# Kernel optimization log

Measured on AMD Instinct MI355X. Metric: run time of the kernel, lower is better.

Reference implementation:

```python
import jax, jax.numpy as jnp
import numpy as np

T, B, D, H = 128, 256, 1024, 150  # seq_len, batch, input feat, lstm hidden (bidir out = 2H = 300)


def _lstm_dir(x, Wih, Whh, b):
    # x: [T,Bn,in]; Wih: [4H,in]; Whh: [4H,H]; b: [4H]. PyTorch gate order i,f,g,o.
    xW = jnp.einsum('tbi,gi->tbg', x, Wih) + b
    Bn = x.shape[1]
    init = (jnp.zeros((Bn, H), x.dtype), jnp.zeros((Bn, H), x.dtype))
    def step(carry, xg):
        h, c = carry
        g = xg + h @ Whh.T
        i, f, gg, o = jnp.split(g, 4, axis=-1)
        c = jax.nn.sigmoid(f) * c + jax.nn.sigmoid(i) * jnp.tanh(gg)
        h = jax.nn.sigmoid(o) * jnp.tanh(c)
        return (h, c), h
    _, hs = jax.lax.scan(step, init, xW)
    return hs


def _bidir(x, Wih, Whh, b):
    fwd = _lstm_dir(x, Wih[0], Whh[0], b[0])
    bwd = _lstm_dir(x[::-1], Wih[1], Whh[1], b[1])[::-1]
    return jnp.concatenate([fwd, bwd], axis=-1)


def _bilstm2(x, Wih0, Whh0, b0, Wih1, Whh1, b1):
    # 2-layer bidirectional LSTM (eval mode, dropout off)
    h = _bidir(x, Wih0, Whh0, b0)
    return _bidir(h, Wih1, Whh1, b1)


def setup_inputs() -> dict:
    key = jax.random.key(0)
    ks = iter(jax.random.split(key, 32))
    U = jax.random.normal(next(ks), (T, B, D), jnp.float32)
    speaker = jax.random.randint(next(ks), (T, B), 0, 2)
    qmask = jax.nn.one_hot(speaker, 2, dtype=jnp.int32)  # [T,B,2] speaker one-hot
    umask = jnp.ones((T, B), jnp.float32)
    seq_lengths = jnp.full((B,), T, dtype=jnp.int32)
    def w(shape):
        return jax.random.normal(next(ks), shape, jnp.float32) * 0.05
    inp = dict(U=U, qmask=qmask, umask=umask, seq_lengths=seq_lengths)
    for pfx in ('rnn', 'pr'):
        inp[pfx + '_Wih0'] = w((2, 4 * H, D))
        inp[pfx + '_Whh0'] = w((2, 4 * H, H))
        inp[pfx + '_b0'] = w((2, 4 * H))
        inp[pfx + '_Wih1'] = w((2, 4 * H, 2 * H))
        inp[pfx + '_Whh1'] = w((2, 4 * H, H))
        inp[pfx + '_b1'] = w((2, 4 * H))
    return inp


def reference(U, qmask, umask, seq_lengths, rnn_Wih0, rnn_Whh0, rnn_b0, rnn_Wih1, rnn_Whh1, rnn_b1, pr_Wih0, pr_Whh0, pr_b0, pr_Wih1, pr_Whh1, pr_b1):
    speaker = jnp.argmax(qmask, axis=-1)  # [T,B] party id of each utterance
    # position of utterance t within its party's compacted sequence
    pos = jnp.take_along_axis(jnp.cumsum(qmask, axis=0), speaker[..., None], axis=-1)[..., 0] - 1  # [T,B]
    bidx = jnp.broadcast_to(jnp.arange(B)[None, :], (T, B))
    # scatter utterances into per-party sequences: [2,T,B,D]
    U_parties = jnp.zeros((2, T, B, D), U.dtype).at[speaker, pos, bidx].set(U)
    xp = jnp.concatenate([U_parties[0], U_parties[1]], axis=1)  # [T,2B,D]
    Ep = _bilstm2(xp, pr_Wih0, pr_Whh0, pr_b0, pr_Wih1, pr_Whh1, pr_b1)  # [T,2B,2H]
    Ep = jnp.stack([Ep[:, :B], Ep[:, B:]], axis=0)  # [2,T,B,2H]
    U_p = Ep[speaker, pos, bidx]  # gather back to dialogue order, [T,B,2H]
    emotions = _bilstm2(U, rnn_Wih0, rnn_Whh0, rnn_b0, rnn_Wih1, rnn_Whh1, rnn_b1)  # [T,B,2H]
    return (emotions + U_p) * umask[..., None]
```

## Files before the change

### kernel.cpp

```cpp
#include <hip/hip_runtime.h>
#include <hip/hip_bf16.h>
#include <math.h>

#define T_ 128
#define B_ 256
#define BP 512
#define D_ 1024
#define H_ 150
#define G_ 600
#define O_ 300
#define ROWS 16
#define NT_ 38
#define KT_ 5
#define KTX 10
#define KAP 40
#define HSTR 168
#define GST 620
#define TPB 512
#define EIT 5
#define NTB 38

typedef float v4f    __attribute__((ext_vector_type(4)));
typedef short bf16x8 __attribute__((ext_vector_type(8)));
typedef float f32x4  __attribute__((ext_vector_type(4)));
typedef unsigned int u32x4 __attribute__((ext_vector_type(4)));
union HU { u32x4 u; bf16x8 h; };

static const size_t N_INV   = 0;
static const size_t N_WPK   = 65536;
static const size_t N_BW1   = N_WPK + 778240;
static const size_t N_HPK   = N_BW1 + 778240;
static const size_t N_X     = N_HPK + 31457280;
static const size_t N_TOTAL = N_X + 78643200 + 256;

static const size_t WPS      = (size_t)NT_ * KT_ * 2 * 512;
static const size_t BW1_STR  = (size_t)KTX * NTB * 2 * 512;
static const size_t BW0_STR  = 32ull * NTB * 2 * 512;
static const size_t RNN_PL   = 2048ull * KAP * 128;
static const size_t PR_PL    = 4096ull * KAP * 128;

static const size_t INV_OFF   = 0;
static const size_t WIHT0_OFF = 65536;
static const size_t WIHT1_OFF = WIHT0_OFF + 4ull * 1024 * 600;
static const size_t WPK_OFF   = WIHT1_OFF + 4ull * 300 * 600;
static const size_t WPK_WORDS = 8ull * NT_ * KT_ * 2 * 512 / 2;
static const size_t XW_OFF    = WPK_OFF + WPK_WORDS;
static const size_t XSLOT     = 32768ull * 600;
static size_t hrnn_off(int nslots) { return XW_OFF + (size_t)nslots * XSLOT; }
static size_t hpr_off(int nslots)  { return hrnn_off(nslots) + 32768ull * 300; }

__device__ __forceinline__ float fsig(float x) {
    return __builtin_amdgcn_rcpf(1.f + __expf(-x));
}
__device__ __forceinline__ float ftanh(float x) {
    float xc = fminf(fmaxf(x, -15.f), 15.f);
    float e = __expf(-2.f * xc);
    return (1.f - e) * __builtin_amdgcn_rcpf(1.f + e);
}

__global__ void k_pos(const int* __restrict__ qmask, int* __restrict__ inv) {
    int b = threadIdx.x;
    for (int p = 0; p < T_; ++p) {
        inv[p * BP + b] = -1;
        inv[p * BP + B_ + b] = -1;
    }
    int c0 = 0, c1 = 0;
    for (int t = 0; t < T_; ++t) {
        int s = qmask[(t * B_ + b) * 2 + 1];
        int p = s ? c1++ : c0++;
        inv[p * BP + s * B_ + b] = t * B_ + b;
    }
}

__global__ void k_zero(unsigned int* __restrict__ p, int n4) {
    int gid = blockIdx.x * 256 + threadIdx.x;
    if (gid < n4) *(u32x4*)(p + (size_t)gid * 4) = (u32x4){0, 0, 0, 0};
}

__global__ void k_transpose(const float* __restrict__ src, float* __restrict__ dst,
                            int K) {
    int idx = blockIdx.x * 256 + threadIdx.x;
    int total = K * G_;
    if (idx < total) {
        int k = idx / G_, g = idx - k * G_;
        dst[idx] = src[(size_t)g * K + k];
    }
}

struct PackArgs { const float* whh[8]; };
__global__ void k_pack(PackArgs pa, unsigned short* __restrict__ wpk) {
    int gid = blockIdx.x * 256 + threadIdx.x;
    int lane = gid & 63;
    int q = gid >> 6;
    int kt = q % KT_; q /= KT_;
    int nt = q % NT_; q /= NT_;
    if (q >= 8) return;
    const float* W = pa.whh[q];
    int col = nt * 16 + (lane & 15);
    int kbase = kt * 32 + (lane >> 4) * 8;
    size_t base = ((((size_t)q * NT_ + nt) * KT_ + kt) * 2) * 512 + (size_t)lane * 8;
    for (int j = 0; j < 8; ++j) {
        int k = kbase + j;
        float v = (col < G_ && k < H_) ? W[(size_t)col * H_ + k] : 0.f;
        unsigned u = __float_as_uint(v);
        unsigned short hi = (unsigned short)(u >> 16);
        float hf = __uint_as_float(u & 0xffff0000u);
        unsigned short lo = (unsigned short)(__float_as_uint(v - hf) >> 16);
        wpk[base + j] = hi;
        wpk[base + 512 + j] = lo;
    }
}

__global__ void k_packB(const float* __restrict__ W, int K, int KT,
                        unsigned short* __restrict__ out) {
    int gid = blockIdx.x * 256 + threadIdx.x;
    int lane = gid & 63, q = gid >> 6;
    int kt = q % KT, nt = q / KT;
    if (nt >= NTB) return;
    int col = nt * 16 + (lane & 15);
    int kb = kt * 32 + (lane >> 4) * 8;
    size_t base = ((size_t)(kt * NTB + nt) * 2) * 512 + (size_t)lane * 8;
    bf16x8 h8 = {0, 0, 0, 0, 0, 0, 0, 0};
    bf16x8 l8 = {0, 0, 0, 0, 0, 0, 0, 0};
#pragma unroll
    for (int j = 0; j < 8; ++j) {
        int k = kb + j;
        float v = (col < G_ && k < K) ? W[(size_t)col * K + k] : 0.f;
        unsigned u = __float_as_uint(v);
        h8[j] = (short)(u >> 16);
        float hf = __uint_as_float(u & 0xffff0000u);
        l8[j] = (short)(__float_as_uint(v - hf) >> 16);
    }
    *(bf16x8*)(out + base) = h8;
    *(bf16x8*)(out + base + 512) = l8;
}

__global__ void k_packU(const float* __restrict__ A, unsigned short* __restrict__ hi,
                        unsigned short* __restrict__ lo) {
    int gid = blockIdx.x * 256 + threadIdx.x;
    int kc = gid & 127, rr = gid >> 7;
    const float* ap = A + (size_t)rr * 1024 + kc * 8;
    size_t off = ((size_t)((rr >> 4) * 128 + kc) * 16 + (rr & 15)) * 8;
    bf16x8 h8, l8;
#pragma unroll
    for (int j = 0; j < 8; ++j) {
        float v = ap[j];
        unsigned u = __float_as_uint(v);
        h8[j] = (short)(u >> 16);
        float hf = __uint_as_float(u & 0xffff0000u);
        l8[j] = (short)(__float_as_uint(v - hf) >> 16);
    }
    *(bf16x8*)(hi + off) = h8;
    *(bf16x8*)(lo + off) = l8;
}

#define LOADK(kt_, S)                                                          \
  {                                                                            \
    if (MODE == 0) {                                                           \
      _Pragma("unroll") for (int mi = 0; mi < 4; ++mi) {                       \
        size_t aoff = ((size_t)((m0 >> 4) + mi) * KA + (kt_) * 4 + quad);      \
        aoff = (aoff * 16 + col16) * 8;                                        \
        a_h##S[mi] = *(const bf16x8*)(Ahi + aoff);                             \
        a_l##S[mi] = *(const bf16x8*)(Alo + aoff);                             \
      }                                                                        \
    } else {                                                                   \
      _Pragma("unroll") for (int mi = 0; mi < 4; ++mi) {                       \
        const unsigned int* ap =                                               \
            Aw + (size_t)(m0 + mi * 16 + col16) * KA + (kt_) * 32 + quad * 8;  \
        u32x4 w0 = *(const u32x4*)ap;                                          \
        u32x4 w1 = *(const u32x4*)(ap + 4);                                    \
        HU hh, ll;                                                             \
        hh.u.x = (w0.x >> 16) | (w0.y & 0xffff0000u);                          \
        hh.u.y = (w0.z >> 16) | (w0.w & 0xffff0000u);                          \
        hh.u.z = (w1.x >> 16) | (w1.y & 0xffff0000u);                          \
        hh.u.w = (w1.z >> 16) | (w1.w & 0xffff0000u);                          \
        ll.u.x = (w0.x & 0xffffu) | (w0.y << 16);                              \
        ll.u.y = (w0.z & 0xffffu) | (w0.w << 16);                              \
        ll.u.z = (w1.x & 0xffffu) | (w1.y << 16);                              \
        ll.u.w = (w1.z & 0xffffu) | (w1.w << 16);                              \
        a_h##S[mi] = hh.h;                                                     \
        a_l##S[mi] = ll.h;                                                     \
      }                                                                        \
    }                                                                          \
    _Pragma("unroll") for (int ni = 0; ni < 4; ++ni) {                         \
      if (bnv[ni]) {                                                           \
        size_t bo = ((size_t)((kt_) * NTB + nt0 + ni) * 2) * 512 + lane * 8;   \
        b_h##S[ni] = *(const bf16x8*)(Bpk + bo);                               \
        b_l##S[ni] = *(const bf16x8*)(Bpk + bo + 512);                         \
      }                                                                        \
    }                                                                          \
  }

#define MMK(S)                                                                 \
  _Pragma("unroll") for (int mi = 0; mi < 4; ++mi)                             \
    _Pragma("unroll") for (int ni = 0; ni < 4; ++ni) {                         \
      acc[mi][ni] = __builtin_amdgcn_mfma_f32_16x16x32_bf16(                   \
          a_h##S[mi], b_h##S[ni], acc[mi][ni], 0, 0, 0);                       \
      acc[mi][ni] = __builtin_amdgcn_mfma_f32_16x16x32_bf16(                   \
          a_h##S[mi], b_l##S[ni], acc[mi][ni], 0, 0, 0);                       \
      acc[mi][ni] = __builtin_amdgcn_mfma_f32_16x16x32_bf16(                   \
          a_l##S[mi], b_h##S[ni], acc[mi][ni], 0, 0, 0);                       \
    }

template<int MODE, int KTN, int KA>
__global__ __launch_bounds__(256) void k_mgemm(const unsigned short* __restrict__ Ahi,
                                               const unsigned short* __restrict__ Alo,
                                               const unsigned int* __restrict__ Aw,
                                               const unsigned short* __restrict__ Bpk,
                                               const float* __restrict__ bias,
                                               float* __restrict__ C) {
    int tid = threadIdx.x, lane = tid & 63, wv = tid >> 6;
    int col16 = lane & 15, quad = lane >> 4;
    int n0 = blockIdx.x * 128 + (wv & 1) * 64;
    int m0 = blockIdx.y * 128 + (wv >> 1) * 64;
    int nt0 = n0 >> 4;

    bool bnv[4]; float bs[4];
#pragma unroll
    for (int ni = 0; ni < 4; ++ni) {
        int nt = nt0 + ni;
        bnv[ni] = (nt < NTB);
        int cc = nt * 16 + col16;
        bs[ni] = (cc < G_) ? bias[cc] : 0.f;
    }

    f32x4 acc[4][4];
#pragma unroll
    for (int mi = 0; mi < 4; ++mi)
#pragma unroll
        for (int ni = 0; ni < 4; ++ni) acc[mi][ni] = (f32x4){0.f, 0.f, 0.f, 0.f};

    bf16x8 z8 = {0, 0, 0, 0, 0, 0, 0, 0};
    bf16x8 a_h0[4], a_l0[4], b_h0[4], b_l0[4];
    bf16x8 a_h1[4], a_l1[4], b_h1[4], b_l1[4];
#pragma unroll
    for (int ni = 0; ni < 4; ++ni) {
        b_h0[ni] = z8; b_l0[ni] = z8; b_h1[ni] = z8; b_l1[ni] = z8;
    }

    LOADK(0, 0);
#pragma unroll 1
    for (int kt = 0; kt < KTN; kt += 2) {
        LOADK(kt + 1, 1);
        MMK(0);
        if (kt + 2 < KTN) { LOADK(kt + 2, 0); }
        MMK(1);
    }

#pragma unroll
    for (int mi = 0; mi < 4; ++mi)
#pragma unroll
        for (int ni = 0; ni < 4; ++ni) {
            int col = n0 + ni * 16 + col16;
            if (col < G_) {
#pragma unroll
                for (int p = 0; p < 4; ++p)
                    C[(size_t)(m0 + mi * 16 + quad * 4 + p) * G_ + col] =
                        acc[mi][ni][p] + bs[ni];
            }
        }
}

__global__ __launch_bounds__(256) void k_gemm(const float* __restrict__ A,
                                              const float* __restrict__ BT,
                                              const float* __restrict__ bias,
                                              float* __restrict__ C,
                                              int M, int K) {
    __shared__ __align__(16) float As[16][136];
    __shared__ __align__(16) float Bs[16][68];
    int n0 = blockIdx.x * 64, m0 = blockIdx.y * 128;
    int tid = threadIdx.x;
    int tx = tid & 15, ty = tid >> 4;
    int ar = tid >> 2, ac = (tid & 3) * 4;
    int kr = tid >> 4, nc = (tid & 15) * 4;
    float acc[8][4];
#pragma unroll
    for (int i = 0; i < 8; ++i)
#pragma unroll
        for (int j = 0; j < 4; ++j) acc[i][j] = 0.f;

    for (int k0 = 0; k0 < K; k0 += 16) {
        bool fullK = (k0 + 16 <= K);
#pragma unroll
        for (int half = 0; half < 2; ++half) {
            int m = m0 + ar + half * 64;
            const float* ap = A + (size_t)m * K + k0 + ac;
            if (fullK) {
                v4f v = *(const v4f*)ap;
                As[ac + 0][ar + half * 64] = v.x;
                As[ac + 1][ar + half * 64] = v.y;
                As[ac + 2][ar + half * 64] = v.z;
                As[ac + 3][ar + half * 64] = v.w;
            } else {
#pragma unroll
                for (int i = 0; i < 4; ++i) {
                    int k = k0 + ac + i;
                    As[ac + i][ar + half * 64] = (k < K) ? ap[i] : 0.f;
                }
            }
        }
        {
            int k = k0 + kr, n = n0 + nc;
            if (fullK && n + 3 < G_) {
                v4f v = *(const v4f*)(BT + (size_t)k * G_ + n);
                Bs[kr][nc + 0] = v.x; Bs[kr][nc + 1] = v.y;
                Bs[kr][nc + 2] = v.z; Bs[kr][nc + 3] = v.w;
            } else {
#pragma unroll
                for (int i = 0; i < 4; ++i) {
                    int nn = n + i;
                    Bs[kr][nc + i] = (k < K && nn < G_) ? BT[(size_t)k * G_ + nn] : 0.f;
                }
            }
        }
        __syncthreads();
#pragma unroll
        for (int kk = 0; kk < 16; ++kk) {
            v4f a0 = *(const v4f*)&As[kk][ty * 8];
            v4f a1 = *(const v4f*)&As[kk][ty * 8 + 4];
            v4f b  = *(const v4f*)&Bs[kk][tx * 4];
            const float* af = (const float*)&a0;
            const float* af2 = (const float*)&a1;
            const float* bf = (const float*)&b;
#pragma unroll
            for (int i = 0; i < 4; ++i)
#pragma unroll
                for (int j = 0; j < 4; ++j) {
                    acc[i][j] += af[i] * bf[j];
                    acc[4 + i][j] += af2[i] * bf[j];
                }
        }
        __syncthreads();
    }
    int n = n0 + tx * 4;
    if (n + 3 < G_) {
        v4f bv = *(const v4f*)(bias + n);
#pragma unroll
        for (int i = 0; i < 8; ++i) {
            int m = m0 + ty * 8 + i;
            v4f o = {acc[i][0] + bv.x, acc[i][1] + bv.y, acc[i][2] + bv.z, acc[i][3] + bv.w};
            *(v4f*)(C + (size_t)m * G_ + n) = o;
        }
    } else {
#pragma unroll
        for (int i = 0; i < 8; ++i) {
            int m = m0 + ty * 8 + i;
#pragma unroll
            for (int j = 0; j < 4; ++j)
                if (n + j < G_) C[(size_t)m * G_ + n + j] = acc[i][j] + bias[n + j];
        }
    }
}

struct Combo0 {
    const float* xw;
    const unsigned short* wpk;
    const float* bias;
    unsigned short* phi;
    unsigned short* plo;
    int Bn, colOff, bwd, gIn;
};
struct Scan0Args { Combo0 c[4]; const int* inv; int blkStart[5]; };

__global__ __launch_bounds__(TPB) void k_scan0(Scan0Args args) {
    int bx = blockIdx.x, ci = 0;
#pragma unroll
    for (int i = 1; i < 4; ++i)
        if (bx >= args.blkStart[i]) ci = i;
    Combo0 cb = args.c[ci];
    int row0 = (bx - args.blkStart[ci]) * ROWS;

    __shared__ __align__(16) unsigned short hsh[ROWS * HSTR];
    __shared__ __align__(16) unsigned short hsl[ROWS * HSTR];
    __shared__ float cs[ROWS * 152];
    __shared__ float gs[ROWS * GST];
    int tid = threadIdx.x;
    int lane = tid & 63, wv = tid >> 6;
    int col16 = lane & 15, quad = lane >> 4;
    for (int i = tid; i < ROWS * HSTR; i += TPB) { hsh[i] = 0; hsl[i] = 0; }
    for (int i = tid; i < ROWS * 152; i += TPB) cs[i] = 0.f;
    __syncthreads();

    int er[EIT], ej[EIT];
#pragma unroll
    for (int it = 0; it < EIT; ++it) {
        int i = tid + it * TPB;
        er[it] = i / 160;
        ej[it] = i - er[it] * 160;
    }

    for (int s = 0; s < T_; ++s) {
        int t = cb.bwd ? (T_ - 1 - s) : s;

        float xi[EIT], xf_[EIT], xg[EIT], xo[EIT];
#pragma unroll
        for (int it = 0; it < EIT; ++it) {
            int r = er[it], j = ej[it];
            const float* xr;
            if (cb.gIn) {
                int g = args.inv[t * cb.Bn + row0 + r];
                xr = (g >= 0) ? cb.xw + (size_t)g * G_ : cb.bias;
            } else {
                xr = cb.xw + ((size_t)t * cb.Bn + row0 + r) * G_;
            }
            bool act = (j < H_);
            xi[it]  = act ? xr[j] : 0.f;
            xf_[it] = act ? xr[H_ + j] : 0.f;
            xg[it]  = act ? xr[2 * H_ + j] : 0.f;
            xo[it]  = act ? xr[3 * H_ + j] : 0.f;
        }

        bf16x8 ahi[KT_], alo[KT_];
#pragma unroll
        for (int kt = 0; kt < KT_; ++kt) {
            int off = col16 * HSTR + kt * 32 + quad * 8;
            ahi[kt] = *(const bf16x8*)&hsh[off];
            alo[kt] = *(const bf16x8*)&hsl[off];
        }

        for (int nt = wv; nt < NT_; nt += 8) {
            f32x4 a0 = {0.f, 0.f, 0.f, 0.f};
            f32x4 a1 = {0.f, 0.f, 0.f, 0.f};
            const bf16x8* bp = (const bf16x8*)cb.wpk + ((size_t)nt * KT_) * 2 * 64 + lane;
#pragma unroll
            for (int kt = 0; kt < KT_; ++kt) {
                bf16x8 bhi = bp[0];
                bf16x8 blo = bp[64];
                bp += 128;
                if (kt < 3) {
                    a0 = __builtin_amdgcn_mfma_f32_16x16x32_bf16(ahi[kt], bhi, a0, 0, 0, 0);
                    a0 = __builtin_amdgcn_mfma_f32_16x16x32_bf16(ahi[kt], blo, a0, 0, 0, 0);
                    a0 = __builtin_amdgcn_mfma_f32_16x16x32_bf16(alo[kt], bhi, a0, 0, 0, 0);
                } else {
                    a1 = __builtin_amdgcn_mfma_f32_16x16x32_bf16(ahi[kt], bhi, a1, 0, 0, 0);
                    a1 = __builtin_amdgcn_mfma_f32_16x16x32_bf16(ahi[kt], blo, a1, 0, 0, 0);
                    a1 = __builtin_amdgcn_mfma_f32_16x16x32_bf16(alo[kt], bhi, a1, 0, 0, 0);
                }
            }
            f32x4 acc = a0 + a1;
#pragma unroll
            for (int p = 0; p < 4; ++p)
                gs[(quad * 4 + p) * GST + nt * 16 + col16] = acc[p];
        }
        __syncthreads();

        size_t mb = ((size_t)t * cb.Bn + row0) >> 4;
#pragma unroll
        for (int it = 0; it < EIT; ++it) {
            int r = er[it], j = ej[it];
            if (j < H_) {
                float gi = gs[r * GST + j] + xi[it];
                float gf = gs[r * GST + H_ + j] + xf_[it];
                float gg = gs[r * GST + 2 * H_ + j] + xg[it];
                float go = gs[r * GST + 3 * H_ + j] + xo[it];
                float ii = fsig(gi), ff = fsig(gf), oo = fsig(go);
                float cc = ff * cs[r * 152 + j] + ii * ftanh(gg);
                float hh = oo * ftanh(cc);
                cs[r * 152 + j] = cc;
                unsigned u = __float_as_uint(hh);
                unsigned short hi16 = (unsigned short)(u >> 16);
                float hf = __uint_as_float(u & 0xffff0000u);
                unsigned short lo16 = (unsigned short)(__float_as_uint(hh - hf) >> 16);
                hsh[r * HSTR + j] = hi16;
                hsl[r * HSTR + j] = lo16;
                int k = cb.colOff + j;
                size_t off = (mb * KAP + (k >> 3)) * 128 + (size_t)r * 8 + (k & 7);
                cb.phi[off] = hi16;
                cb.plo[off] = lo16;
            }
        }
        __syncthreads();
    }
}

struct Combo1 {
    const unsigned short* xphi;
    const unsigned short* xplo;
    const unsigned short* whh;
    const unsigned short* wih;
    const float* bias;
    float* out;
    int Bn, colOff, bwd, gOut;
};
struct Scan1Args {
    Combo1 c[4];
    const int* inv;
    unsigned char mci[96];
    unsigned char mrb[96];
};

__global__ __launch_bounds__(TPB) void k_scan1(Scan1Args args) {
    int bx = blockIdx.x;
    int ci = args.mci[bx];
    Combo1 cb = args.c[ci];
    int row0 = (int)args.mrb[bx] * ROWS;

    __shared__ __align__(16) unsigned short hsh[ROWS * HSTR];
    __shared__ __align__(16) unsigned short hsl[ROWS * HSTR];
    __shared__ float cs[ROWS * 152];
    __shared__ float gs[ROWS * GST];
    int tid = threadIdx.x;
    int lane = tid & 63, wv = tid >> 6;
    int col16 = lane & 15, quad = lane >> 4;
    for (int i = tid; i < ROWS * HSTR; i += TPB) { hsh[i] = 0; hsl[i] = 0; }
    for (int i = tid; i < ROWS * 152; i += TPB) cs[i] = 0.f;
    __syncthreads();

    int er[EIT], ej[EIT];
    float bxi[EIT], bxf[EIT], bxg[EIT], bxo[EIT];
#pragma unroll
    for (int it = 0; it < EIT; ++it) {
        int i = tid + it * TPB;
        er[it] = i / 160;
        ej[it] = i - er[it] * 160;
        int j = ej[it];
        bool act = (j < H_);
        bxi[it] = act ? cb.bias[j] : 0.f;
        bxf[it] = act ? cb.bias[H_ + j] : 0.f;
        bxg[it] = act ? cb.bias[2 * H_ + j] : 0.f;
        bxo[it] = act ? cb.bias[3 * H_ + j] : 0.f;
    }

    for (int s = 0; s < T_; ++s) {
        int t = cb.bwd ? (T_ - 1 - s) : s;
        size_t mb = ((size_t)t * cb.Bn + row0) >> 4;

        bf16x8 xh[KTX], xl[KTX];
#pragma unroll
        for (int kt = 0; kt < KTX; ++kt) {
            size_t off = (mb * KAP + kt * 4 + quad) * 128 + (size_t)col16 * 8;
            xh[kt] = *(const bf16x8*)(cb.xphi + off);
            xl[kt] = *(const bf16x8*)(cb.xplo + off);
        }

        bf16x8 ahi[KT_], alo[KT_];
#pragma unroll
        for (int kt = 0; kt < KT_; ++kt) {
            int off = col16 * HSTR + kt * 32 + quad * 8;
            ahi[kt] = *(const bf16x8*)&hsh[off];
            alo[kt] = *(const bf16x8*)&hsl[off];
        }

        for (int nt = wv; nt < NT_; nt += 8) {
            f32x4 a0 = {0.f, 0.f, 0.f, 0.f};
            f32x4 a1 = {0.f, 0.f, 0.f, 0.f};
            const bf16x8* bp = (const bf16x8*)cb.whh + ((size_t)nt * KT_) * 2 * 64 + lane;
#pragma unroll
            for (int kt = 0; kt < KT_; ++kt) {
                bf16x8 bhi = bp[0];
                bf16x8 blo = bp[64];
                bp += 128;
                if (kt < 3) {
                    a0 = __builtin_amdgcn_mfma_f32_16x16x32_bf16(ahi[kt], bhi, a0, 0, 0, 0);
                    a0 = __builtin_amdgcn_mfma_f32_16x16x32_bf16(ahi[kt], blo, a0, 0, 0, 0);
                    a0 = __builtin_amdgcn_mfma_f32_16x16x32_bf16(alo[kt], bhi, a0, 0, 0, 0);
                } else {
                    a1 = __builtin_amdgcn_mfma_f32_16x16x32_bf16(ahi[kt], bhi, a1, 0, 0, 0);
                    a1 = __builtin_amdgcn_mfma_f32_16x16x32_bf16(ahi[kt], blo, a1, 0, 0, 0);
                    a1 = __builtin_amdgcn_mfma_f32_16x16x32_bf16(alo[kt], bhi, a1, 0, 0, 0);
                }
            }
#pragma unroll
            for (int kt = 0; kt < KTX; ++kt) {
                const bf16x8* xp = (const bf16x8*)cb.wih + ((size_t)(kt * NTB + nt) * 2) * 64 + lane;
                bf16x8 bhi = xp[0];
                bf16x8 blo = xp[64];
                if (kt & 1) {
                    a1 = __builtin_amdgcn_mfma_f32_16x16x32_bf16(xh[kt], bhi, a1, 0, 0, 0);
                    a1 = __builtin_amdgcn_mfma_f32_16x16x32_bf16(xh[kt], blo, a1, 0, 0, 0);
                    a1 = __builtin_amdgcn_mfma_f32_16x16x32_bf16(xl[kt], bhi, a1, 0, 0, 0);
                } else {
                    a0 = __builtin_amdgcn_mfma_f32_16x16x32_bf16(xh[kt], bhi, a0, 0, 0, 0);
                    a0 = __builtin_amdgcn_mfma_f32_16x16x32_bf16(xh[kt], blo, a0, 0, 0, 0);
                    a0 = __builtin_amdgcn_mfma_f32_16x16x32_bf16(xl[kt], bhi, a0, 0, 0, 0);
                }
            }
            f32x4 acc = a0 + a1;
#pragma unroll
            for (int p = 0; p < 4; ++p)
                gs[(quad * 4 + p) * GST + nt * 16 + col16] = acc[p];
        }
        __syncthreads();

#pragma unroll
        for (int it = 0; it < EIT; ++it) {
            int r = er[it], j = ej[it];
            if (j < H_) {
                float gi = gs[r * GST + j] + bxi[it];
                float gf = gs[r * GST + H_ + j] + bxf[it];
                float gg = gs[r * GST + 2 * H_ + j] + bxg[it];
                float go = gs[r * GST + 3 * H_ + j] + bxo[it];
                float ii = fsig(gi), ff = fsig(gf), oo = fsig(go);
                float cc = ff * cs[r * 152 + j] + ii * ftanh(gg);
                float hh = oo * ftanh(cc);
                cs[r * 152 + j] = cc;
                unsigned u = __float_as_uint(hh);
                hsh[r * HSTR + j] = (unsigned short)(u >> 16);
                float hf = __uint_as_float(u & 0xffff0000u);
                hsl[r * HSTR + j] = (unsigned short)(__float_as_uint(hh - hf) >> 16);
                if (cb.gOut) {
                    int g = args.inv[t * cb.Bn + row0 + r];
                    if (g >= 0)
                        cb.out[(size_t)g * O_ + cb.colOff + j] = hh;
                } else {
                    cb.out[((size_t)t * cb.Bn + row0 + r) * O_ + cb.colOff + j] = hh;
                }
            }
        }
        __syncthreads();
    }
}

__global__ void k_add(float* __restrict__ out, const float* __restrict__ up,
                      const float* __restrict__ um) {
    int idx = blockIdx.x * 256 + threadIdx.x;
    if (idx < T_ * B_ * O_)
        out[idx] = (out[idx] + up[idx]) * um[idx / O_];
}

struct Combo {
    const float* xw;
    const unsigned short* wpk;
    const float* bias;
    float* out;
    int Bn, colOff, bwd, gIn, gOut;
};
struct ScanArgs {
    Combo c[4];
    const int* inv;
    const float* addSrc;
    const float* umask;
    int blkStart[5];
};

__global__ __launch_bounds__(TPB) void k_scan(ScanArgs args) {
    int bx = blockIdx.x, ci = 0;
#pragma unroll
    for (int i = 1; i < 4; ++i)
        if (bx >= args.blkStart[i]) ci = i;
    Combo cb = args.c[ci];
    int row0 = (bx - args.blkStart[ci]) * ROWS;

    __shared__ __align__(16) unsigned short hsh[ROWS * HSTR];
    __shared__ __align__(16) unsigned short hsl[ROWS * HSTR];
    __shared__ float cs[ROWS * 152];
    __shared__ float gs[ROWS * GST];
    int tid = threadIdx.x;
    int lane = tid & 63, wv = tid >> 6;
    int col16 = lane & 15, quad = lane >> 4;
    for (int i = tid; i < ROWS * HSTR; i += TPB) { hsh[i] = 0; hsl[i] = 0; }
    for (int i = tid; i < ROWS * 152; i += TPB) cs[i] = 0.f;
    __syncthreads();

    int er[EIT], ej[EIT];
#pragma unroll
    for (int it = 0; it < EIT; ++it) {
        int i = tid + it * TPB;
        er[it] = i / 160;
        ej[it] = i - er[it] * 160;
    }

    for (int s = 0; s < T_; ++s) {
        int t = cb.bwd ? (T_ - 1 - s) : s;

        float xi[EIT], xf_[EIT], xg[EIT], xo[EIT];
#pragma unroll
        for (int it = 0; it < EIT; ++it) {
            int r = er[it], j = ej[it];
            const float* xr;
            if (cb.gIn) {
                int g = args.inv[t * cb.Bn + row0 + r];
                xr = (g >= 0) ? cb.xw + (size_t)g * G_ : cb.bias;
            } else {
                xr = cb.xw + ((size_t)t * cb.Bn + row0 + r) * G_;
            }
            bool act = (j < H_);
            xi[it]  = act ? xr[j] : 0.f;
            xf_[it] = act ? xr[H_ + j] : 0.f;
            xg[it]  = act ? xr[2 * H_ + j] : 0.f;
            xo[it]  = act ? xr[3 * H_ + j] : 0.f;
        }

        bf16x8 ahi[KT_], alo[KT_];
#pragma unroll
        for (int kt = 0; kt < KT_; ++kt) {
            int off = col16 * HSTR + kt * 32 + quad * 8;
            ahi[kt] = *(const bf16x8*)&hsh[off];
            alo[kt] = *(const bf16x8*)&hsl[off];
        }

        for (int nt = wv; nt < NT_; nt += 8) {
            f32x4 a0 = {0.f, 0.f, 0.f, 0.f};
            f32x4 a1 = {0.f, 0.f, 0.f, 0.f};
            const bf16x8* bp = (const bf16x8*)cb.wpk + ((size_t)nt * KT_) * 2 * 64 + lane;
#pragma unroll
            for (int kt = 0; kt < KT_; ++kt) {
                bf16x8 bhi = bp[0];
                bf16x8 blo = bp[64];
                bp += 128;
                if (kt < 3) {
                    a0 = __builtin_amdgcn_mfma_f32_16x16x32_bf16(ahi[kt], bhi, a0, 0, 0, 0);
                    a0 = __builtin_amdgcn_mfma_f32_16x16x32_bf16(ahi[kt], blo, a0, 0, 0, 0);
                    a0 = __builtin_amdgcn_mfma_f32_16x16x32_bf16(alo[kt], bhi, a0, 0, 0, 0);
                } else {
                    a1 = __builtin_amdgcn_mfma_f32_16x16x32_bf16(ahi[kt], bhi, a1, 0, 0, 0);
                    a1 = __builtin_amdgcn_mfma_f32_16x16x32_bf16(ahi[kt], blo, a1, 0, 0, 0);
                    a1 = __builtin_amdgcn_mfma_f32_16x16x32_bf16(alo[kt], bhi, a1, 0, 0, 0);
                }
            }
            f32x4 acc = a0 + a1;
#pragma unroll
            for (int p = 0; p < 4; ++p)
                gs[(quad * 4 + p) * GST + nt * 16 + col16] = acc[p];
        }
        __syncthreads();

#pragma unroll
        for (int it = 0; it < EIT; ++it) {
            int r = er[it], j = ej[it];
            if (j < H_) {
                float gi = gs[r * GST + j] + xi[it];
                float gf = gs[r * GST + H_ + j] + xf_[it];
                float gg = gs[r * GST + 2 * H_ + j] + xg[it];
                float go = gs[r * GST + 3 * H_ + j] + xo[it];
                float ii = fsig(gi), ff = fsig(gf), oo = fsig(go);
                float cc = ff * cs[r * 152 + j] + ii * ftanh(gg);
                float hh = oo * ftanh(cc);
                cs[r * 152 + j] = cc;
                unsigned u = __float_as_uint(hh);
                hsh[r * HSTR + j] = (unsigned short)(u >> 16);
                float hf = __uint_as_float(u & 0xffff0000u);
                hsl[r * HSTR + j] = (unsigned short)(__float_as_uint(hh - hf) >> 16);
                if (cb.gOut) {
                    int g = args.inv[t * cb.Bn + row0 + r];
                    if (g >= 0) {
                        size_t o = (size_t)g * O_ + cb.colOff + j;
                        if (args.addSrc)
                            cb.out[o] = (args.addSrc[o] + hh) * args.umask[g];
                        else
                            cb.out[o] = hh;
                    }
                } else {
                    cb.out[((size_t)t * cb.Bn + row0 + r) * O_ + cb.colOff + j] = hh;
                }
            }
        }
        __syncthreads();
    }
}

extern "C" void kernel_launch(void* const* d_in, const int* in_sizes, int n_in,
                              void* d_out, int out_size, void* d_ws, size_t ws_size,
                              hipStream_t stream) {
    const float* U        = (const float*)d_in[0];
    const int*   qmask    = (const int*)d_in[1];
    const float* umask    = (const float*)d_in[2];
    const float* rnn_Wih0 = (const float*)d_in[4];
    const float* rnn_Whh0 = (const float*)d_in[5];
    const float* rnn_b0   = (const float*)d_in[6];
    const float* rnn_Wih1 = (const float*)d_in[7];
    const float* rnn_Whh1 = (const float*)d_in[8];
    const float* rnn_b1   = (const float*)d_in[9];
    const float* pr_Wih0  = (const float*)d_in[10];
    const float* pr_Whh0  = (const float*)d_in[11];
    const float* pr_b0    = (const float*)d_in[12];
    const float* pr_Wih1  = (const float*)d_in[13];
    const float* pr_Whh1  = (const float*)d_in[14];
    const float* pr_b1    = (const float*)d_in[15];

    float* ws = (float*)d_ws;
    dim3 blk(256);
    dim3 sblk(TPB);
    const int INF = 0x7fffffff;

    PackArgs pa;
    for (int d = 0; d < 2; ++d) {
        pa.whh[0 + d] = rnn_Whh0 + (size_t)d * G_ * H_;
        pa.whh[2 + d] = pr_Whh0  + (size_t)d * G_ * H_;
        pa.whh[4 + d] = rnn_Whh1 + (size_t)d * G_ * H_;
        pa.whh[6 + d] = pr_Whh1  + (size_t)d * G_ * H_;
    }
    int packLanes = 8 * NT_ * KT_ * 64;

    if (ws_size >= N_TOTAL * 4ull) {
        int*   inv   = (int*)d_ws + N_INV;
        unsigned short* wpk = (unsigned short*)(ws + N_WPK);
        unsigned short* bw1 = (unsigned short*)(ws + N_BW1);
        unsigned short* hpk = (unsigned short*)(ws + N_HPK);
        unsigned short* rnnHi = hpk;
        unsigned short* rnnLo = rnnHi + RNN_PL;
        unsigned short* prHi  = rnnLo + RNN_PL;
        unsigned short* prLo  = prHi + PR_PL;
        unsigned short* bw0 = hpk;
        unsigned short* Uhi = hpk + 4 * BW0_STR;
        unsigned short* Ulo = Uhi + 16777216ull;
        float* X[4];
        for (int i = 0; i < 4; ++i) X[i] = ws + N_X + (size_t)i * 19660800ull;
        float* Uptmp = X[0];

        k_pos<<<dim3(1), dim3(256), 0, stream>>>(qmask, inv);
        k_pack<<<dim3((packLanes + 255) / 256), dim3(256), 0, stream>>>(pa, wpk);

        const float* W1p[4] = {rnn_Wih1, rnn_Wih1 + (size_t)G_ * O_,
                               pr_Wih1,  pr_Wih1 + (size_t)G_ * O_};
        {
            int lanes = KTX * NTB * 64;
            for (int g = 0; g < 4; ++g)
                k_packB<<<dim3((lanes + 255) / 256), blk, 0, stream>>>(
                    W1p[g], O_, KTX, bw1 + (size_t)g * BW1_STR);
        }

        const float* W0p[4] = {rnn_Wih0, rnn_Wih0 + (size_t)G_ * D_,
                               pr_Wih0,  pr_Wih0 + (size_t)G_ * D_};
        const float* b0p[4] = {rnn_b0, rnn_b0 + G_, pr_b0, pr_b0 + G_};
        {
            int lanes = 32 * NTB * 64;
            for (int g = 0; g < 4; ++g)
                k_packB<<<dim3((lanes + 255) / 256), blk, 0, stream>>>(
                    W0p[g], D_, 32, bw0 + (size_t)g * BW0_STR);
        }

        dim3 gm0(5, 128);
        for (int half = 0; half < 2; ++half) {
            k_packU<<<dim3(8192), blk, 0, stream>>>(U + (size_t)half * 16384 * D_, Uhi, Ulo);
            for (int g = 0; g < 4; ++g)
                k_mgemm<0, 32, 128><<<gm0, blk, 0, stream>>>(
                    Uhi, Ulo, nullptr, bw0 + (size_t)g * BW0_STR, b0p[g],
                    X[g] + (size_t)half * 16384 * G_);
        }

        k_zero<<<dim3((31457280 / 4 + 255) / 256), blk, 0, stream>>>(
            (unsigned int*)hpk, 31457280 / 4);

        Scan0Args sa = {};
        sa.inv = inv;
        auto set0 = [&](int i, const float* xw, int wslot, const float* bi,
                        unsigned short* phi, unsigned short* plo,
                        int Bn, int co, int bw, int gi) {
            sa.c[i].xw = xw; sa.c[i].wpk = wpk + (size_t)wslot * WPS;
            sa.c[i].bias = bi; sa.c[i].phi = phi; sa.c[i].plo = plo;
            sa.c[i].Bn = Bn; sa.c[i].colOff = co; sa.c[i].bwd = bw; sa.c[i].gIn = gi;
        };
        set0(0, X[0], 0, nullptr, rnnHi, rnnLo, B_, 0, 0, 0);
        set0(1, X[1], 1, nullptr, rnnHi, rnnLo, B_, H_, 1, 0);
        set0(2, X[2], 2, pr_b0 + 0 * G_, prHi, prLo, BP, 0, 0, 1);
        set0(3, X[3], 3, pr_b0 + 1 * G_, prHi, prLo, BP, H_, 1, 1);
        sa.blkStart[0] = 0; sa.blkStart[1] = 16; sa.blkStart[2] = 32;
        sa.blkStart[3] = 64; sa.blkStart[4] = 96;
        k_scan0<<<dim3(96), sblk, 0, stream>>>(sa);

        Scan1Args sm = {};
        sm.inv = inv;
        auto set1 = [&](int i, const unsigned short* xh, const unsigned short* xl,
                        int wslot, int bslot, const float* bi, float* o,
                        int Bn, int co, int bw, int go) {
            sm.c[i].xphi = xh; sm.c[i].xplo = xl;
            sm.c[i].whh = wpk + (size_t)wslot * WPS;
            sm.c[i].wih = bw1 + (size_t)bslot * BW1_STR;
            sm.c[i].bias = bi; sm.c[i].out = o;
            sm.c[i].Bn = Bn; sm.c[i].colOff = co; sm.c[i].bwd = bw; sm.c[i].gOut = go;
        };
        set1(0, rnnHi, rnnLo, 4, 0, rnn_b1 + 0 * G_, (float*)d_out, B_, 0, 0, 0);
        set1(1, rnnHi, rnnLo, 5, 1, rnn_b1 + 1 * G_, (float*)d_out, B_, H_, 1, 0);
        set1(2, prHi, prLo, 6, 2, pr_b1 + 0 * G_, Uptmp, BP, 0, 0, 1);
        set1(3, prHi, prLo, 7, 3, pr_b1 + 1 * G_, Uptmp, BP, H_, 1, 1);
        {
            static const unsigned char laneAssign[8][12] = {
                {0,0,0,0,0,0,0,0,0,0,0,0},
                {0,0,0,0,1,1,1,1,1,1,1,1},
                {1,1,1,1,1,1,1,1,2,2,2,2},
                {2,2,2,2,2,2,2,2,2,2,2,2},
                {2,2,2,2,2,2,2,2,2,2,2,2},
                {2,2,2,2,3,3,3,3,3,3,3,3},
                {3,3,3,3,3,3,3,3,3,3,3,3},
                {3,3,3,3,3,3,3,3,3,3,3,3},
            };
            int cnt[4] = {0, 0, 0, 0};
            for (int lanex = 0; lanex < 8; ++lanex)
                for (int slot = 0; slot < 12; ++slot) {
                    int bxx = lanex + 8 * slot;
                    int c = laneAssign[lanex][slot];
                    sm.mci[bxx] = (unsigned char)c;
                    sm.mrb[bxx] = (unsigned char)cnt[c]++;
                }
        }
        k_scan1<<<dim3(96), sblk, 0, stream>>>(sm);

        k_add<<<dim3((T_ * B_ * O_ + 255) / 256), dim3(256), 0, stream>>>(
            (float*)d_out, Uptmp, umask);
        return;
    }

    int*   inv   = (int*)d_ws + INV_OFF;
    float* wihT0 = ws + WIHT0_OFF;
    float* wihT1 = ws + WIHT1_OFF;
    unsigned short* wpk = (unsigned short*)(ws + WPK_OFF);
    float* X0    = ws + XW_OFF;
    float* X1    = X0 + XSLOT;
    float* h_rnn = ws + hrnn_off(2);
    float* h_pr  = ws + hpr_off(2);

    const size_t W0S = 1024ull * 600, W1S = 300ull * 600;

    k_pos<<<dim3(1), dim3(256), 0, stream>>>(qmask, inv);
    auto TP = [&](const float* src, float* dst, int K) {
        int total = K * G_;
        k_transpose<<<dim3((total + 255) / 256), dim3(256), 0, stream>>>(src, dst, K);
    };
    for (int d = 0; d < 2; ++d) {
        TP(rnn_Wih0 + (size_t)d * G_ * D_, wihT0 + (0 + d) * W0S, D_);
        TP(pr_Wih0  + (size_t)d * G_ * D_, wihT0 + (2 + d) * W0S, D_);
        TP(rnn_Wih1 + (size_t)d * G_ * O_, wihT1 + (0 + d) * W1S, O_);
        TP(pr_Wih1  + (size_t)d * G_ * O_, wihT1 + (2 + d) * W1S, O_);
    }
    k_pack<<<dim3((packLanes + 255) / 256), dim3(256), 0, stream>>>(pa, wpk);

    ScanArgs z = {};
    auto setCombo = [&](ScanArgs& s2, int i, const float* xw, int wslot,
                        const float* bi, float* o, int Bn, int co, int bw,
                        int gi, int go) {
        s2.c[i].xw = xw; s2.c[i].wpk = wpk + (size_t)wslot * WPS;
        s2.c[i].bias = bi; s2.c[i].out = o;
        s2.c[i].Bn = Bn; s2.c[i].colOff = co; s2.c[i].bwd = bw;
        s2.c[i].gIn = gi; s2.c[i].gOut = go;
    };

    dim3 g32k(10, 256), g64k(10, 512);
    for (int d = 0; d < 2; ++d) {
        k_gemm<<<g32k, blk, 0, stream>>>(U, wihT0 + (0 + d) * W0S, rnn_b0 + d * G_, X0, 32768, D_);
        k_gemm<<<g32k, blk, 0, stream>>>(U, wihT0 + (2 + d) * W0S, pr_b0 + d * G_, X1, 32768, D_);
        ScanArgs sa = z;
        sa.inv = inv;
        setCombo(sa, 0, X0, 0 + d, nullptr, h_rnn, B_, d * H_, d, 0, 0);
        setCombo(sa, 1, X1, 2 + d, pr_b0 + d * G_, h_pr, BP, d * H_, d, 1, 0);
        sa.blkStart[0] = 0; sa.blkStart[1] = 16; sa.blkStart[2] = INF;
        sa.blkStart[3] = INF; sa.blkStart[4] = 48;
        k_scan<<<dim3(48), sblk, 0, stream>>>(sa);
    }
    k_gemm<<<g32k, blk, 0, stream>>>(h_rnn, wihT1 + 0 * W1S, rnn_b1 + 0 * G_, X0, 32768, O_);
    k_gemm<<<g32k, blk, 0, stream>>>(h_rnn, wihT1 + 1 * W1S, rnn_b1 + 1 * G_, X1, 32768, O_);
    {
        ScanArgs sr = z;
        sr.inv = inv;
        setCombo(sr, 0, X0, 4, nullptr, h_rnn, B_, 0, 0, 0, 0);
        setCombo(sr, 1, X1, 5, nullptr, h_rnn, B_, H_, 1, 0, 0);
        sr.blkStart[0] = 0; sr.blkStart[1] = 16; sr.blkStart[2] = INF;
        sr.blkStart[3] = INF; sr.blkStart[4] = 32;
        k_scan<<<dim3(32), sblk, 0, stream>>>(sr);
    }
    for (int d = 0; d < 2; ++d) {
        k_gemm<<<g64k, blk, 0, stream>>>(h_pr, wihT1 + (2 + d) * W1S, pr_b1 + d * G_, X0, 65536, O_);
        ScanArgs sp = z;
        sp.inv = inv; sp.addSrc = h_rnn; sp.umask = umask;
        setCombo(sp, 0, X0, 6 + d, nullptr, (float*)d_out, BP, d * H_, d, 0, 1);
        sp.blkStart[0] = 0; sp.blkStart[1] = INF; sp.blkStart[2] = INF;
        sp.blkStart[3] = INF; sp.blkStart[4] = 32;
        k_scan<<<dim3(32), sblk, 0, stream>>>(sp);
    }
}
```

Baseline: 3.733 ms.

## Process two timesteps per iteration in scan1, staging x tiles through LDS

Restructures the layer-1 recurrent scan so each iteration handles two timesteps. The input projections for both steps are computed together, so every Wih fragment loaded from global memory feeds two timesteps. The x tiles for the next pair are staged cooperatively into a 40KB shared buffer, overlapping with the second step's gate update. This halves Wih traffic and hoists x loads off the critical path, but adds LDS pressure that may lower occupancy and more accumulator registers.

```diff
diff --git a/kernel.cpp b/kernel.cpp
--- a/kernel.cpp
+++ b/kernel.cpp
@@ -499,12 +499,14 @@
     __shared__ __align__(16) unsigned short hsl[ROWS * HSTR];
     __shared__ float cs[ROWS * 152];
     __shared__ float gs[ROWS * GST];
+    __shared__ __align__(16) unsigned int xstg[10240];
+    unsigned short* xstgS = (unsigned short*)xstg;
+
     int tid = threadIdx.x;
     int lane = tid & 63, wv = tid >> 6;
     int col16 = lane & 15, quad = lane >> 4;
     for (int i = tid; i < ROWS * HSTR; i += TPB) { hsh[i] = 0; hsl[i] = 0; }
     for (int i = tid; i < ROWS * 152; i += TPB) cs[i] = 0.f;
-    __syncthreads();
 
     int er[EIT], ej[EIT];
     float bxi[EIT], bxf[EIT], bxg[EIT], bxo[EIT];
@@ -521,67 +523,24 @@
         bxo[it] = act ? cb.bias[3 * H_ + j] : 0.f;
     }
 
-    for (int s = 0; s < T_; ++s) {
-        int t = cb.bwd ? (T_ - 1 - s) : s;
-        size_t mb = ((size_t)t * cb.Bn + row0) >> 4;
-
-        bf16x8 xh[KTX], xl[KTX];
-#pragma unroll
-        for (int kt = 0; kt < KTX; ++kt) {
-            size_t off = (mb * KAP + kt * 4 + quad) * 128 + (size_t)col16 * 8;
-            xh[kt] = *(const bf16x8*)(cb.xphi + off);
-            xl[kt] = *(const bf16x8*)(cb.xplo + off);
-        }
-
-        bf16x8 ahi[KT_], alo[KT_];
-#pragma unroll
-        for (int kt = 0; kt < KT_; ++kt) {
-            int off = col16 * HSTR + kt * 32 + quad * 8;
-            ahi[kt] = *(const bf16x8*)&hsh[off];
-            alo[kt] = *(const bf16x8*)&hsl[off];
-        }
-
-        for (int nt = wv; nt < NT_; nt += 8) {
-            f32x4 a0 = {0.f, 0.f, 0.f, 0.f};
-            f32x4 a1 = {0.f, 0.f, 0.f, 0.f};
-            const bf16x8* bp = (const bf16x8*)cb.whh + ((size_t)nt * KT_) * 2 * 64 + lane;
-#pragma unroll
-            for (int kt = 0; kt < KT_; ++kt) {
-                bf16x8 bhi = bp[0];
-                bf16x8 blo = bp[64];
-                bp += 128;
-                if (kt < 3) {
-                    a0 = __builtin_amdgcn_mfma_f32_16x16x32_bf16(ahi[kt], bhi, a0, 0, 0, 0);
-                    a0 = __builtin_amdgcn_mfma_f32_16x16x32_bf16(ahi[kt], blo, a0, 0, 0, 0);
-                    a0 = __builtin_amdgcn_mfma_f32_16x16x32_bf16(alo[kt], bhi, a0, 0, 0, 0);
-                } else {
-                    a1 = __builtin_amdgcn_mfma_f32_16x16x32_bf16(ahi[kt], bhi, a1, 0, 0, 0);
-                    a1 = __builtin_amdgcn_mfma_f32_16x16x32_bf16(ahi[kt], blo, a1, 0, 0, 0);
-                    a1 = __builtin_amdgcn_mfma_f32_16x16x32_bf16(alo[kt], bhi, a1, 0, 0, 0);
-                }
-            }
-#pragma unroll
-            for (int kt = 0; kt < KTX; ++kt) {
-                const bf16x8* xp = (const bf16x8*)cb.wih + ((size_t)(kt * NTB + nt) * 2) * 64 + lane;
-                bf16x8 bhi = xp[0];
-                bf16x8 blo = xp[64];
-                if (kt & 1) {
-                    a1 = __builtin_amdgcn_mfma_f32_16x16x32_bf16(xh[kt], bhi, a1, 0, 0, 0);
-                    a1 = __builtin_amdgcn_mfma_f32_16x16x32_bf16(xh[kt], blo, a1, 0, 0, 0);
-                    a1 = __builtin_amdgcn_mfma_f32_16x16x32_bf16(xl[kt], bhi, a1, 0, 0, 0);
-                } else {
-                    a0 = __builtin_amdgcn_mfma_f32_16x16x32_bf16(xh[kt], bhi, a0, 0, 0, 0);
-                    a0 = __builtin_amdgcn_mfma_f32_16x16x32_bf16(xh[kt], blo, a0, 0, 0, 0);
-                    a0 = __builtin_amdgcn_mfma_f32_16x16x32_bf16(xl[kt], bhi, a0, 0, 0, 0);
-                }
-            }
-            f32x4 acc = a0 + a1;
-#pragma unroll
-            for (int p = 0; p < 4; ++p)
-                gs[(quad * 4 + p) * GST + nt * 16 + col16] = acc[p];
-        }
-        __syncthreads();
-
+    auto stage = [&](int tA, int tB) {
+        size_t mbA = ((size_t)tA * cb.Bn + row0) >> 4;
+        size_t mbB = ((size_t)tB * cb.Bn + row0) >> 4;
+        int reg = tid >> 7, lt = tid & 127;
+        const unsigned int* src;
+        if (reg == 0)      src = (const unsigned int*)cb.xphi + mbA * 2560;
+        else if (reg == 1) src = (const unsigned int*)cb.xplo + mbA * 2560;
+        else if (reg == 2) src = (const unsigned int*)cb.xphi + mbB * 2560;
+        else               src = (const unsigned int*)cb.xplo + mbB * 2560;
+        unsigned int* d = xstg + reg * 2560;
+#pragma unroll
+        for (int k = 0; k < 5; ++k) {
+            int o = (lt + k * 128) * 4;
+            *(u32x4*)(d + o) = *(const u32x4*)(src + o);
+        }
+    };
+
+    auto update = [&](int t) {
 #pragma unroll
         for (int it = 0; it < EIT; ++it) {
             int r = er[it], j = ej[it];
@@ -607,6 +566,118 @@
                 }
             }
         }
+    };
+
+    {
+        int t0 = cb.bwd ? (T_ - 1) : 0;
+        int t1 = cb.bwd ? (T_ - 2) : 1;
+        stage(t0, t1);
+    }
+    __syncthreads();
+
+    f32x4 accS[5], accX1[5];
+    for (int s = 0; s < T_; s += 2) {
+        int t0 = cb.bwd ? (T_ - 1 - s) : s;
+        int t1 = cb.bwd ? (T_ - 2 - s) : (s + 1);
+
+#pragma unroll
+        for (int i = 0; i < 5; ++i) {
+            accS[i]  = (f32x4){0.f, 0.f, 0.f, 0.f};
+            accX1[i] = (f32x4){0.f, 0.f, 0.f, 0.f};
+        }
+#pragma unroll
+        for (int kt = 0; kt < KTX; ++kt) {
+            int xb = kt * 512 + quad * 128 + col16 * 8;
+            bf16x8 x0h = *(const bf16x8*)&xstgS[xb];
+            bf16x8 x0l = *(const bf16x8*)&xstgS[5120 + xb];
+            bf16x8 x1h = *(const bf16x8*)&xstgS[10240 + xb];
+            bf16x8 x1l = *(const bf16x8*)&xstgS[15360 + xb];
+#pragma unroll
+            for (int i = 0; i < 5; ++i) {
+                int nt = wv + i * 8;
+                if (nt < NT_) {
+                    const bf16x8* xp = (const bf16x8*)cb.wih +
+                                       ((size_t)(kt * NTB + nt) * 2) * 64 + lane;
+                    bf16x8 bhi = xp[0];
+                    bf16x8 blo = xp[64];
+                    accS[i]  = __builtin_amdgcn_mfma_f32_16x16x32_bf16(x0h, bhi, accS[i], 0, 0, 0);
+                    accS[i]  = __builtin_amdgcn_mfma_f32_16x16x32_bf16(x0h, blo, accS[i], 0, 0, 0);
+                    accS[i]  = __builtin_amdgcn_mfma_f32_16x16x32_bf16(x0l, bhi, accS[i], 0, 0, 0);
+                    accX1[i] = __builtin_amdgcn_mfma_f32_16x16x32_bf16(x1h, bhi, accX1[i], 0, 0, 0);
+                    accX1[i] = __builtin_amdgcn_mfma_f32_16x16x32_bf16(x1h, blo, accX1[i], 0, 0, 0);
+                    accX1[i] = __builtin_amdgcn_mfma_f32_16x16x32_bf16(x1l, bhi, accX1[i], 0, 0, 0);
+                }
+            }
+        }
+#pragma unroll
+        for (int kt = 0; kt < KT_; ++kt) {
+            int off = col16 * HSTR + kt * 32 + quad * 8;
+            bf16x8 ah = *(const bf16x8*)&hsh[off];
+            bf16x8 al = *(const bf16x8*)&hsl[off];
+#pragma unroll
+            for (int i = 0; i < 5; ++i) {
+                int nt = wv + i * 8;
+                if (nt < NT_) {
+                    const bf16x8* bp = (const bf16x8*)cb.whh +
+                                       ((size_t)(nt * KT_ + kt) * 2) * 64 + lane;
+                    bf16x8 bhi = bp[0];
+                    bf16x8 blo = bp[64];
+                    accS[i] = __builtin_amdgcn_mfma_f32_16x16x32_bf16(ah, bhi, accS[i], 0, 0, 0);
+                    accS[i] = __builtin_amdgcn_mfma_f32_16x16x32_bf16(ah, blo, accS[i], 0, 0, 0);
+                    accS[i] = __builtin_amdgcn_mfma_f32_16x16x32_bf16(al, bhi, accS[i], 0, 0, 0);
+                }
+            }
+        }
+#pragma unroll
+        for (int i = 0; i < 5; ++i) {
+            int nt = wv + i * 8;
+            if (nt < NT_) {
+#pragma unroll
+                for (int p = 0; p < 4; ++p)
+                    gs[(quad * 4 + p) * GST + nt * 16 + col16] = accS[i][p];
+            }
+        }
+        __syncthreads();
+
+        update(t0);
+        __syncthreads();
+
+#pragma unroll
+        for (int kt = 0; kt < KT_; ++kt) {
+            int off = col16 * HSTR + kt * 32 + quad * 8;
+            bf16x8 ah = *(const bf16x8*)&hsh[off];
+            bf16x8 al = *(const bf16x8*)&hsl[off];
+#pragma unroll
+            for (int i = 0; i < 5; ++i) {
+                int nt = wv + i * 8;
+                if (nt < NT_) {
+                    const bf16x8* bp = (const bf16x8*)cb.whh +
+                                       ((size_t)(nt * KT_ + kt) * 2) * 64 + lane;
+                    bf16x8 bhi = bp[0];
+                    bf16x8 blo = bp[64];
+                    accX1[i] = __builtin_amdgcn_mfma_f32_16x16x32_bf16(ah, bhi, accX1[i], 0, 0, 0);
+                    accX1[i] = __builtin_amdgcn_mfma_f32_16x16x32_bf16(ah, blo, accX1[i], 0, 0, 0);
+                    accX1[i] = __builtin_amdgcn_mfma_f32_16x16x32_bf16(al, bhi, accX1[i], 0, 0, 0);
+                }
+            }
+        }
+#pragma unroll
+        for (int i = 0; i < 5; ++i) {
+            int nt = wv + i * 8;
+            if (nt < NT_) {
+#pragma unroll
+                for (int p = 0; p < 4; ++p)
+                    gs[(quad * 4 + p) * GST + nt * 16 + col16] = accX1[i][p];
+            }
+        }
+        __syncthreads();
+
+        if (s + 2 < T_) {
+            int n0 = cb.bwd ? (T_ - 3 - s) : (s + 2);
+            int n1 = cb.bwd ? (T_ - 4 - s) : (s + 3);
+            stage(n0, n1);
+        }
+        update(t1);
         __syncthreads();
     }
 }
```

Result: slower. 5.542 ms (+48.5%).
